# Performance work log

Hardware: AMD Instinct MI355X
Metric: run time of the kernel (lower is better)

## Reference

```python
import jax, jax.numpy as jnp
import numpy as np
import math

DIM = 2048
NUM_HEADS = 32
HEAD_DIM = DIM // NUM_HEADS  # 64; HEAD_DIM//2 == NUM_HEADS (required by original rope broadcasting)
SEQ_LEN = 2048
BATCH = 2
ROPE_BASE = 10000.0


def apply_rope(inputs, positions):
    # Faithful to original: positions is [L]; sinusoid broadcasts to [1, L, H/2, 1]
    # and then multiplies [B, L, N, H/2] -- the original code relies on N == H/2.
    head_dim = inputs.shape[-1]
    fraction = 2.0 * jnp.arange(head_dim // 2, dtype=inputs.dtype) / head_dim
    timescale = ROPE_BASE ** fraction                      # [H/2]
    sinusoid = positions[:, None] / timescale[None, None, :]  # [1, L, H/2]
    sinusoid = sinusoid[..., None]                         # [1, L, H/2, 1]
    sin = jnp.sin(sinusoid)
    cos = jnp.cos(sinusoid)
    first, second = jnp.split(inputs, 2, axis=-1)          # each [B, L, N, H/2]
    return jnp.concatenate([first * cos - second * sin,
                            second * cos + first * sin], axis=-1)


def setup_inputs() -> dict:
    key = jax.random.key(0)
    ks = jax.random.split(key, 9)
    s = 0.02
    inp = {
        'x': jax.random.normal(ks[0], (BATCH, SEQ_LEN, DIM), dtype=jnp.float32),
        'wq_w': jax.random.normal(ks[1], (DIM, DIM), dtype=jnp.float32) * s,
        'wq_b': jnp.zeros((DIM,), dtype=jnp.float32),
        'wk_w': jax.random.normal(ks[2], (DIM, DIM), dtype=jnp.float32) * s,
        'wk_b': jnp.zeros((DIM,), dtype=jnp.float32),
        'wv_w': jax.random.normal(ks[3], (DIM, DIM), dtype=jnp.float32) * s,
        'wv_b': jnp.zeros((DIM,), dtype=jnp.float32),
        'wo_w': jax.random.normal(ks[4], (DIM, DIM), dtype=jnp.float32) * s,
        'wo_b': jnp.zeros((DIM,), dtype=jnp.float32),
    }
    return inp


def reference(x, wq_w, wq_b, wk_w, wk_b, wv_w, wv_b, wo_w, wo_b):
    B, L, _ = x.shape
    N, H = NUM_HEADS, HEAD_DIM
    q = (x @ wq_w.T + wq_b).reshape(B, L, N, H)
    k = (x @ wk_w.T + wk_b).reshape(B, L, N, H)
    v = (x @ wv_w.T + wv_b).reshape(B, L, N, H)
    positions = jnp.arange(L, dtype=x.dtype)
    q = apply_rope(q, positions)
    k = apply_rope(k, positions)
    # [B, N, L, H]
    q = q.transpose(0, 2, 1, 3)
    k = k.transpose(0, 2, 1, 3)
    v = v.transpose(0, 2, 1, 3)
    scale = math.sqrt(H)
    scores = jnp.einsum('bnqh,bnkh->bnqk', q, k) / scale   # [B, N, L, L]
    causal = jnp.tril(jnp.ones((L, L), dtype=bool))
    scores = jnp.where(causal[None, None], scores, -jnp.inf)
    attn = jax.nn.softmax(scores, axis=-1)
    context = jnp.einsum('bnqk,bnkh->bnqh', attn, v)        # [B, N, L, H]
    context = context.transpose(0, 2, 1, 3).reshape(B, L, DIM)
    return context @ wo_w.T + wo_b
```

## Files before the change

### kernel.cpp

```cpp
#include <hip/hip_runtime.h>
#include <stdint.h>

#define D_MODEL 2048
#define SEQLEN  2048

typedef float f32x4  __attribute__((ext_vector_type(4)));
typedef float f32x16 __attribute__((ext_vector_type(16)));
typedef int   i32x4  __attribute__((ext_vector_type(4)));
typedef short s16x4  __attribute__((ext_vector_type(4)));
typedef __bf16 bf16x8 __attribute__((ext_vector_type(8)));

__device__ __forceinline__ unsigned short f2bf(float f) {
  union { float f; uint32_t u; } x; x.f = f;
  uint32_t r = (x.u + 0x7FFFu + ((x.u >> 16) & 1u)) >> 16;
  return (unsigned short)r;
}

__device__ __forceinline__ uint32_t cvtpk(float lo, float hi) {
  uint32_t r;
  asm("v_cvt_pk_bf16_f32 %0, %1, %2" : "=v"(r) : "v"(lo), "v"(hi));
  return r;
}

__device__ __forceinline__ bf16x8 as_bf16x8(i32x4 v) {
  union { i32x4 i; bf16x8 b; } u; u.i = v; return u.b;
}

#define MFMA16(acc, a, b) \
  acc = __builtin_amdgcn_mfma_f32_16x16x32_bf16(as_bf16x8(a), as_bf16x8(b), acc, 0, 0, 0)
#define MFMA32(acc, a, b) \
  acc = __builtin_amdgcn_mfma_f32_32x32x16_bf16(as_bf16x8(a), as_bf16x8(b), acc, 0, 0, 0)

__device__ __forceinline__ void gload16(const void* g, void* lds) {
  __builtin_amdgcn_global_load_lds(
      (const __attribute__((address_space(1))) unsigned int*)(uintptr_t)g,
      (__attribute__((address_space(3))) unsigned int*)(uint32_t)(uintptr_t)lds,
      16, 0, 0);
}

__global__ void cvt_all_k(const float* __restrict__ x,
                          const float* __restrict__ w0, const float* __restrict__ w1,
                          const float* __restrict__ w2, const float* __restrict__ w3,
                          unsigned short* __restrict__ xo,
                          unsigned short* __restrict__ o0, unsigned short* __restrict__ o1,
                          unsigned short* __restrict__ o2, unsigned short* __restrict__ o3) {
  const int i = blockIdx.x * 256 + threadIdx.x;
  const float* src; unsigned short* dst; int off;
  if (i < 2097152) { src = x; dst = xo; off = i; }
  else {
    const int j = i - 2097152, seg = j >> 20;
    off = j & 1048575;
    src = seg == 0 ? w0 : seg == 1 ? w1 : seg == 2 ? w2 : w3;
    dst = seg == 0 ? o0 : seg == 1 ? o1 : seg == 2 ? o2 : o3;
  }
  f32x4 v = *(const f32x4*)&src[(size_t)off * 4];
  s16x4 o;
#pragma unroll
  for (int j = 0; j < 4; ++j) o[j] = (short)f2bf(v[j]);
  *(s16x4*)&dst[(size_t)off * 4] = o;
}

template <bool ROPE, bool F32OUT>
__global__ __launch_bounds__(512) void gemm1(
    const unsigned short* __restrict__ A,
    const unsigned short* __restrict__ W,
    const float* __restrict__ bias,
    unsigned short* __restrict__ Ob,
    float* __restrict__ Of) {
  constexpr int PLANE_E = 384 * 32;
  __shared__ alignas(16) unsigned short L[4 * PLANE_E];

  const int t = threadIdx.x;
  const int w = t >> 6, l = t & 63;
  const int wm = w >> 1, wn = w & 1;
  const int band = l >> 4, ln = l & 15;

  const int m0 = blockIdx.y * 256;
  const int nloc = blockIdx.x * 128;

  auto stage1 = [&](int p, int ktile, int b, int i) {
    unsigned short* dst = L + (b * 2 + p) * PLANE_E;
    const int idx = w * 3 + i;
    const int row = idx * 16 + (l >> 2);
    const int gblk = (l & 3) ^ ((row >> 1) & 3);
    const int kcol = ktile * 64 + p * 32;
    const unsigned short* src =
        (idx < 16) ? &A[(size_t)(m0 + row) * D_MODEL + kcol + gblk * 8]
                   : &W[(size_t)(nloc + row - 256) * D_MODEL + kcol + gblk * 8];
    gload16(src, dst + idx * 512);
  };
  auto ld = [&](const unsigned short* pl, int r) {
    return *(const i32x4*)&pl[r * 32 + (((band ^ (r >> 1)) & 3) << 3)];
  };

  f32x4 acc[4][4] = {};

#pragma unroll
  for (int i = 0; i < 3; ++i) stage1(0, 0, 0, i);
#pragma unroll
  for (int i = 0; i < 3; ++i) stage1(1, 0, 0, i);
  asm volatile("s_waitcnt vmcnt(3)" ::: "memory");
  __builtin_amdgcn_s_barrier();

  for (int kt = 0; kt < 32; ++kt) {
    const int rb = kt & 1;
    const int ktn = (kt + 1) & 31;
#pragma unroll
    for (int kh = 0; kh < 2; ++kh) {
      const unsigned short* pl = L + (rb * 2 + kh) * PLANE_E;
      i32x4 bv[4], av[2];
#pragma unroll
      for (int nf = 0; nf < 4; ++nf) bv[nf] = ld(pl, 256 + wn * 64 + nf * 16 + ln);
#pragma unroll
      for (int mf = 0; mf < 2; ++mf) av[mf] = ld(pl, wm * 64 + mf * 16 + ln);
      stage1(kh, ktn, rb ^ 1, 0);
      stage1(kh, ktn, rb ^ 1, 1);
      __builtin_amdgcn_s_barrier();
      asm volatile("s_waitcnt lgkmcnt(0)" ::: "memory");
      __builtin_amdgcn_sched_barrier(0);
      __builtin_amdgcn_s_setprio(1);
#pragma unroll
      for (int mf = 0; mf < 2; ++mf)
#pragma unroll
        for (int nf = 0; nf < 4; ++nf) MFMA16(acc[mf][nf], av[mf], bv[nf]);
      __builtin_amdgcn_s_setprio(0);
      __builtin_amdgcn_s_barrier();
#pragma unroll
      for (int mf = 0; mf < 2; ++mf) av[mf] = ld(pl, wm * 64 + (2 + mf) * 16 + ln);
      stage1(kh, ktn, rb ^ 1, 2);
      __builtin_amdgcn_s_barrier();
      asm volatile("s_waitcnt lgkmcnt(0)" ::: "memory");
      __builtin_amdgcn_sched_barrier(0);
      __builtin_amdgcn_s_setprio(1);
#pragma unroll
      for (int mf = 0; mf < 2; ++mf)
#pragma unroll
        for (int nf = 0; nf < 4; ++nf) MFMA16(acc[2 + mf][nf], av[mf], bv[nf]);
      __builtin_amdgcn_s_setprio(0);
      asm volatile("s_waitcnt vmcnt(3)" ::: "memory");
      __builtin_amdgcn_s_barrier();
    }
  }
  asm volatile("s_waitcnt vmcnt(0)" ::: "memory");

  float bb[4];
#pragma unroll
  for (int nf = 0; nf < 4; ++nf) bb[nf] = bias[nloc + wn * 64 + nf * 16 + ln];

  const int head = (nloc + wn * 64) >> 6;
  const float ts = powf(10000.0f, (float)head * (1.0f / 32.0f));
#pragma unroll
  for (int am = 0; am < 4; ++am) {
#pragma unroll
    for (int r = 0; r < 4; ++r) {
      const int row = m0 + wm * 64 + am * 16 + band * 4 + r;
      float vals[4];
#pragma unroll
      for (int nf = 0; nf < 4; ++nf) vals[nf] = acc[am][nf][r] + bb[nf];
      if constexpr (ROPE) {
        const float pos = (float)(row & (SEQLEN - 1));
        float sv, cv;
        __sincosf(pos / ts, &sv, &cv);
#pragma unroll
        for (int pp = 0; pp < 2; ++pp) {
          const float f0 = vals[pp], s0 = vals[pp + 2];
          vals[pp]     = f0 * cv - s0 * sv;
          vals[pp + 2] = s0 * cv + f0 * sv;
        }
      }
#pragma unroll
      for (int nf = 0; nf < 4; ++nf) {
        const size_t oi = (size_t)row * D_MODEL + nloc + wn * 64 + nf * 16 + ln;
        if constexpr (F32OUT) Of[oi] = vals[nf];
        else                  Ob[oi] = f2bf(vals[nf]);
      }
    }
  }
}

__global__ __launch_bounds__(256) void attn_fwd(
    const unsigned short* __restrict__ Q, const unsigned short* __restrict__ K,
    const unsigned short* __restrict__ V, unsigned short* __restrict__ O) {
  __shared__ alignas(16) unsigned short Ks[2][64 * 64];
  __shared__ alignas(16) unsigned short Vt[2][64 * 80];

  const int t = threadIdx.x;
  const int w = t >> 6, l = t & 63;
  const int l31 = l & 31, t5 = l >> 5;
  const int bx = blockIdx.x, head = blockIdx.y, b = blockIdx.z;
  const int h0 = head * 64;
  const size_t rb = (size_t)b * SEQLEN;

  const int vg = t & 7, vrow = t >> 3;
  const int kdr = l >> 3, kdb = l & 7;

  for (int pi = 0; pi < 2; ++pi) {
    const int qt = pi ? (15 - bx) : bx;
    const int q0 = qt * 128;
    const int qg = q0 + w * 32 + l31;

    i32x4 qf[4];
#pragma unroll
    for (int hk = 0; hk < 4; ++hk)
      qf[hk] = *(const i32x4*)&Q[(rb + qg) * D_MODEL + h0 + hk * 16 + t5 * 8];

    f32x16 oacc[2] = {};
    float lsum = 0.f;
    const int nkt = qt * 2 + 2;

    {
#pragma unroll
      for (int i = 0; i < 2; ++i) {
        const int drow = (i * 4 + w) * 8 + kdr;
        const int sblk = kdb ^ (drow & 7);
        gload16(&K[(rb + drow) * D_MODEL + h0 + sblk * 8], &Ks[0][(i * 4 + w) * 512]);
      }
      i32x4 vv[2];
#pragma unroll
      for (int i = 0; i < 2; ++i)
        vv[i] = *(const i32x4*)&V[(rb + i * 32 + vrow) * D_MODEL + h0 + vg * 8];
      asm volatile("s_waitcnt vmcnt(0)" ::: "memory");
#pragma unroll
      for (int i = 0; i < 2; ++i) {
        const int r = i * 32 + vrow, c8 = vg * 8;
        union { i32x4 v; unsigned short s[8]; } u; u.v = vv[i];
#pragma unroll
        for (int j = 0; j < 8; ++j) Vt[0][(c8 + j) * 80 + (r ^ c8)] = u.s[j];
      }
    }
    __syncthreads();

    for (int kt = 0; kt < nkt; ++kt) {
      const int cur = kt & 1, nxt = cur ^ 1;
      const int k0 = kt * 64;
      const bool more = (kt + 1 < nkt);

      i32x4 vv[2];
      if (more) {
        const int k1 = k0 + 64;
#pragma unroll
        for (int i = 0; i < 2; ++i) {
          const int drow = (i * 4 + w) * 8 + kdr;
          const int sblk = kdb ^ (drow & 7);
          gload16(&K[(rb + k1 + drow) * D_MODEL + h0 + sblk * 8],
                  &Ks[nxt][(i * 4 + w) * 512]);
        }
#pragma unroll
        for (int i = 0; i < 2; ++i)
          vv[i] = *(const i32x4*)&V[(rb + k1 + i * 32 + vrow) * D_MODEL + h0 + vg * 8];
      }

      f32x16 sacc[2] = {};
#pragma unroll
      for (int kvf = 0; kvf < 2; ++kvf) {
        const int krow = kvf * 32 + l31;
#pragma unroll
        for (int hk = 0; hk < 4; ++hk) {
          i32x4 a = *(const i32x4*)&Ks[cur][krow * 64 + ((2 * hk + t5) ^ (krow & 7)) * 8];
          MFMA32(sacc[kvf], a, qf[hk]);
        }
      }

      const bool needmask = (k0 + 64 > q0 + w * 32);
      uint32_t W[2][4][2];
#pragma unroll
      for (int kvf = 0; kvf < 2; ++kvf)
#pragma unroll
        for (int g = 0; g < 4; ++g)
#pragma unroll
          for (int p = 0; p < 2; ++p) {
            float pv[2];
#pragma unroll
            for (int e = 0; e < 2; ++e) {
              const int reg = 4 * g + 2 * p + e;
              const int kvl = kvf * 32 + 8 * g + 4 * t5 + 2 * p + e;
              pv[e] = __expf(sacc[kvf][reg] * 0.125f);
              if (needmask && (k0 + kvl > qg)) pv[e] = 0.f;
              lsum += pv[e];
            }
            W[kvf][g][p] = cvtpk(pv[0], pv[1]);
          }

#pragma unroll
      for (int ks = 0; ks < 4; ++ks) {
        const int kvf = ks >> 1;
        const int gA = 2 * (ks & 1), gB = gA + 1;
        uint32_t a0 = W[kvf][gA][0], b0 = W[kvf][gB][0];
        uint32_t a1 = W[kvf][gA][1], b1 = W[kvf][gB][1];
        asm("v_permlane32_swap_b32 %0, %1" : "+v"(a0), "+v"(b0));
        asm("v_permlane32_swap_b32 %0, %1" : "+v"(a1), "+v"(b1));
        i32x4 pf;
        pf[0] = (int)a0; pf[1] = (int)a1; pf[2] = (int)b0; pf[3] = (int)b1;
#pragma unroll
        for (int hf = 0; hf < 2; ++hf) {
          const int h = hf * 32 + l31;
          i32x4 vb = *(const i32x4*)&Vt[cur][h * 80 + ((ks * 16 + t5 * 8) ^ ((h >> 3) * 8))];
          MFMA32(oacc[hf], pf, vb);
        }
      }

      if (more) {
        asm volatile("s_waitcnt vmcnt(0)" ::: "memory");
#pragma unroll
        for (int i = 0; i < 2; ++i) {
          const int r = i * 32 + vrow, c8 = vg * 8;
          union { i32x4 v; unsigned short s[8]; } u; u.v = vv[i];
#pragma unroll
          for (int j = 0; j < 8; ++j) Vt[nxt][(c8 + j) * 80 + (r ^ c8)] = u.s[j];
        }
      }
      __syncthreads();
    }

    lsum += __shfl_xor(lsum, 32);
    const float inv = 1.0f / lsum;

#pragma unroll
    for (int g2 = 0; g2 < 4; ++g2)
#pragma unroll
      for (int rr = 0; rr < 4; ++rr) {
        const int rowl = rr + 8 * g2 + 4 * t5;
        const float invr = __shfl(inv, (l & 32) + rowl);
        const size_t gr = rb + q0 + w * 32 + rowl;
#pragma unroll
        for (int hf = 0; hf < 2; ++hf)
          O[gr * D_MODEL + h0 + hf * 32 + l31] = f2bf(oacc[hf][4 * g2 + rr] * invr);
      }
  }
}

extern "C" void kernel_launch(void* const* d_in, const int* in_sizes, int n_in,
                              void* d_out, int out_size, void* d_ws, size_t ws_size,
                              hipStream_t stream) {
  const float* x    = (const float*)d_in[0];
  const float* wq_w = (const float*)d_in[1];
  const float* wq_b = (const float*)d_in[2];
  const float* wk_w = (const float*)d_in[3];
  const float* wk_b = (const float*)d_in[4];
  const float* wv_w = (const float*)d_in[5];
  const float* wv_b = (const float*)d_in[6];
  const float* wo_w = (const float*)d_in[7];
  const float* wo_b = (const float*)d_in[8];
  float* out = (float*)d_out;

  unsigned short* ws  = (unsigned short*)d_ws;
  unsigned short* xb  = ws;
  unsigned short* wqb = xb  + 8388608;
  unsigned short* wkb = wqb + 4194304;
  unsigned short* wvb = wkb + 4194304;
  unsigned short* wob = wvb + 4194304;
  unsigned short* qb  = wob + 4194304;
  unsigned short* kb  = qb  + 8388608;
  unsigned short* vb  = kb  + 8388608;
  unsigned short* cb  = xb;

  cvt_all_k<<<24576, 256, 0, stream>>>(x, wq_w, wk_w, wv_w, wo_w,
                                       xb, wqb, wkb, wvb, wob);

  dim3 g(16, 16);
  gemm1<true,  false><<<g, 512, 0, stream>>>(xb, wqb, wq_b, qb, nullptr);
  gemm1<true,  false><<<g, 512, 0, stream>>>(xb, wkb, wk_b, kb, nullptr);
  gemm1<false, false><<<g, 512, 0, stream>>>(xb, wvb, wv_b, vb, nullptr);

  attn_fwd<<<dim3(8, 32, 2), 256, 0, stream>>>(qb, kb, vb, cb);

  gemm1<false, true><<<g, 512, 0, stream>>>(cb, wob, wo_b, nullptr, out);
}
```

Measured before the change: 264.7 us.

## Load V asynchronously into LDS and read it transposed with ds_read_b64_tr_b16

V tiles no longer pass through registers and get scattered into a padded transposed LDS layout with 16-bit stores. They are now copied straight from global memory into LDS with gload16 in a permuted row order. The PV MFMA operands are then fetched with the hardware transpose-read instruction ds_read_b64_tr_b16, using staged lgkmcnt waits so the reads overlap the softmax work. The exponential is also switched to exp2f with the scale folded in. The aim is to remove the many scalar LDS stores and the register round trip per tile. The risk is that the permuted layout and wait counts must exactly match the MFMA operand layout, or results will be wrong.

```diff
diff --git a/kernel.cpp b/kernel.cpp
--- a/kernel.cpp
+++ b/kernel.cpp
@@ -6,6 +6,7 @@
 
 typedef float f32x4  __attribute__((ext_vector_type(4)));
 typedef float f32x16 __attribute__((ext_vector_type(16)));
+typedef int   i32x2  __attribute__((ext_vector_type(2)));
 typedef int   i32x4  __attribute__((ext_vector_type(4)));
 typedef short s16x4  __attribute__((ext_vector_type(4)));
 typedef __bf16 bf16x8 __attribute__((ext_vector_type(8)));
@@ -182,7 +183,7 @@
     const unsigned short* __restrict__ Q, const unsigned short* __restrict__ K,
     const unsigned short* __restrict__ V, unsigned short* __restrict__ O) {
   __shared__ alignas(16) unsigned short Ks[2][64 * 64];
-  __shared__ alignas(16) unsigned short Vt[2][64 * 80];
+  __shared__ alignas(16) unsigned short Vt[2][64 * 64];
 
   const int t = threadIdx.x;
   const int w = t >> 6, l = t & 63;
@@ -191,8 +192,31 @@
   const int h0 = head * 64;
   const size_t rb = (size_t)b * SEQLEN;
 
-  const int vg = t & 7, vrow = t >> 3;
   const int kdr = l >> 3, kdb = l & 7;
+
+  int vkv[2], vcol[2];
+#pragma unroll
+  for (int i = 0; i < 2; ++i) {
+    const int s = i * 256 + t;
+    const int blk = s >> 6;
+    const int tau = (s >> 3) & 7;
+    vkv[i] = (blk >> 1) * 16 + ((tau >> 1) & 1) * 8 + (tau >> 2) * 4 + ((s & 7) >> 1);
+    vcol[i] = (blk & 1) * 32 + (tau & 1) * 16 + (s & 1) * 8;
+  }
+
+  auto stageKV = [&](int bb2, int kbase) {
+#pragma unroll
+    for (int i = 0; i < 2; ++i) {
+      const int drow = (i * 4 + w) * 8 + kdr;
+      const int sblk = kdb ^ (drow & 7);
+      gload16(&K[(rb + kbase + drow) * D_MODEL + h0 + sblk * 8],
+              &Ks[bb2][(i * 4 + w) * 512]);
+    }
+#pragma unroll
+    for (int i = 0; i < 2; ++i)
+      gload16(&V[(rb + kbase + vkv[i]) * D_MODEL + h0 + vcol[i]],
+              &Vt[bb2][i * 2048 + w * 512]);
+  };
 
   for (int pi = 0; pi < 2; ++pi) {
     const int qt = pi ? (15 - bx) : bx;
@@ -208,26 +232,8 @@
     float lsum = 0.f;
     const int nkt = qt * 2 + 2;
 
-    {
-#pragma unroll
-      for (int i = 0; i < 2; ++i) {
-        const int drow = (i * 4 + w) * 8 + kdr;
-        const int sblk = kdb ^ (drow & 7);
-        gload16(&K[(rb + drow) * D_MODEL + h0 + sblk * 8], &Ks[0][(i * 4 + w) * 512]);
-      }
-      i32x4 vv[2];
-#pragma unroll
-      for (int i = 0; i < 2; ++i)
-        vv[i] = *(const i32x4*)&V[(rb + i * 32 + vrow) * D_MODEL + h0 + vg * 8];
-      asm volatile("s_waitcnt vmcnt(0)" ::: "memory");
-#pragma unroll
-      for (int i = 0; i < 2; ++i) {
-        const int r = i * 32 + vrow, c8 = vg * 8;
-        union { i32x4 v; unsigned short s[8]; } u; u.v = vv[i];
-#pragma unroll
-        for (int j = 0; j < 8; ++j) Vt[0][(c8 + j) * 80 + (r ^ c8)] = u.s[j];
-      }
-    }
+    stageKV(0, 0);
+    asm volatile("s_waitcnt vmcnt(0)" ::: "memory");
     __syncthreads();
 
     for (int kt = 0; kt < nkt; ++kt) {
@@ -235,20 +241,7 @@
       const int k0 = kt * 64;
       const bool more = (kt + 1 < nkt);
 
-      i32x4 vv[2];
-      if (more) {
-        const int k1 = k0 + 64;
-#pragma unroll
-        for (int i = 0; i < 2; ++i) {
-          const int drow = (i * 4 + w) * 8 + kdr;
-          const int sblk = kdb ^ (drow & 7);
-          gload16(&K[(rb + k1 + drow) * D_MODEL + h0 + sblk * 8],
-                  &Ks[nxt][(i * 4 + w) * 512]);
-        }
-#pragma unroll
-        for (int i = 0; i < 2; ++i)
-          vv[i] = *(const i32x4*)&V[(rb + k1 + i * 32 + vrow) * D_MODEL + h0 + vg * 8];
-      }
+      if (more) stageKV(nxt, k0 + 64);
 
       f32x16 sacc[2] = {};
 #pragma unroll
@@ -261,6 +254,21 @@
         }
       }
 
+      i32x2 trr[4][2][2];
+      {
+        const uint32_t vb0 = (uint32_t)(uintptr_t)&Vt[cur][0] + (uint32_t)(l * 8);
+#pragma unroll
+        for (int ks = 0; ks < 4; ++ks)
+#pragma unroll
+          for (int hf = 0; hf < 2; ++hf) {
+            const uint32_t ba = vb0 + (ks * 2 + hf) * 1024;
+            asm volatile("ds_read_b64_tr_b16 %0, %1"
+                         : "=v"(trr[ks][hf][0]) : "v"(ba) : "memory");
+            asm volatile("ds_read_b64_tr_b16 %0, %1"
+                         : "=v"(trr[ks][hf][1]) : "v"(ba + 512) : "memory");
+          }
+      }
+
       const bool needmask = (k0 + 64 > q0 + w * 32);
       uint32_t W[2][4][2];
 #pragma unroll
@@ -274,7 +282,7 @@
             for (int e = 0; e < 2; ++e) {
               const int reg = 4 * g + 2 * p + e;
               const int kvl = kvf * 32 + 8 * g + 4 * t5 + 2 * p + e;
-              pv[e] = __expf(sacc[kvf][reg] * 0.125f);
+              pv[e] = exp2f(sacc[kvf][reg] * 0.18033688f);
               if (needmask && (k0 + kvl > qg)) pv[e] = 0.f;
               lsum += pv[e];
             }
@@ -291,24 +299,21 @@
         asm("v_permlane32_swap_b32 %0, %1" : "+v"(a1), "+v"(b1));
         i32x4 pf;
         pf[0] = (int)a0; pf[1] = (int)a1; pf[2] = (int)b0; pf[3] = (int)b1;
+        if (ks == 0)      asm volatile("s_waitcnt lgkmcnt(12)" ::: "memory");
+        else if (ks == 1) asm volatile("s_waitcnt lgkmcnt(8)"  ::: "memory");
+        else if (ks == 2) asm volatile("s_waitcnt lgkmcnt(4)"  ::: "memory");
+        else              asm volatile("s_waitcnt lgkmcnt(0)"  ::: "memory");
+        __builtin_amdgcn_sched_barrier(0);
 #pragma unroll
         for (int hf = 0; hf < 2; ++hf) {
-          const int h = hf * 32 + l31;
-          i32x4 vb = *(const i32x4*)&Vt[cur][h * 80 + ((ks * 16 + t5 * 8) ^ ((h >> 3) * 8))];
-          MFMA32(oacc[hf], pf, vb);
+          i32x4 vbf;
+          vbf[0] = trr[ks][hf][0][0]; vbf[1] = trr[ks][hf][0][1];
+          vbf[2] = trr[ks][hf][1][0]; vbf[3] = trr[ks][hf][1][1];
+          MFMA32(oacc[hf], pf, vbf);
         }
       }
 
-      if (more) {
-        asm volatile("s_waitcnt vmcnt(0)" ::: "memory");
-#pragma unroll
-        for (int i = 0; i < 2; ++i) {
-          const int r = i * 32 + vrow, c8 = vg * 8;
-          union { i32x4 v; unsigned short s[8]; } u; u.v = vv[i];
-#pragma unroll
-          for (int j = 0; j < 8; ++j) Vt[nxt][(c8 + j) * 80 + (r ^ c8)] = u.s[j];
-        }
-      }
+      if (more) asm volatile("s_waitcnt vmcnt(0)" ::: "memory");
       __syncthreads();
     }
 
```

New measurement: 272.5 us. 2.9% more time.
